# Kernel tuning notes

Measured on AMD Instinct MI355X. Metric: run time of the kernel, lower is better.

## Reference

```python
import jax, jax.numpy as jnp
import numpy as np
import math

HIDDEN, HEADS, D_K = 768, 12, 64
BS, SEQ = 4, 2048


def setup_inputs() -> dict:
    key = jax.random.key(0)
    ks = jax.random.split(key, 5)
    s = 1.0 / math.sqrt(HIDDEN)
    return {
        "x": jax.random.normal(ks[0], (BS, SEQ, HIDDEN), dtype=jnp.float32),
        "Wq": jax.random.normal(ks[1], (HIDDEN, HIDDEN), dtype=jnp.float32) * s,
        "bq": jnp.zeros((HIDDEN,), jnp.float32),
        "Wk": jax.random.normal(ks[2], (HIDDEN, HIDDEN), dtype=jnp.float32) * s,
        "bk": jnp.zeros((HIDDEN,), jnp.float32),
        "Wv": jax.random.normal(ks[3], (HIDDEN, HIDDEN), dtype=jnp.float32) * s,
        "bv": jnp.zeros((HIDDEN,), jnp.float32),
        "Wo": jax.random.normal(ks[4], (HIDDEN, HIDDEN), dtype=jnp.float32) * s,
        "bo": jnp.zeros((HIDDEN,), jnp.float32),
    }


def reference(x, Wq, bq, Wk, bk, Wv, bv, Wo, bo):
    bs, seq, _ = x.shape
    # projections; nn.Linear computes x @ W.T + b
    def proj(W, b):
        y = jnp.einsum("bsd,ed->bse", x, W) + b
        return y.reshape(bs, seq, HEADS, D_K).transpose(0, 2, 1, 3)  # [b,h,s,d]
    q, k, v = proj(Wq, bq), proj(Wk, bk), proj(Wv, bv)
    scores = jnp.einsum("bhqd,bhkd->bhqk", q, k) / jnp.sqrt(jnp.float32(D_K))
    attn = jax.nn.softmax(scores, axis=-1)  # dropout = 0 (eval)
    ctx = jnp.einsum("bhqk,bhkd->bhqd", attn, v)
    ctx = ctx.transpose(0, 2, 1, 3).reshape(bs, seq, HIDDEN)
    return jnp.einsum("bsd,ed->bse", ctx, Wo) + bo
```

## Files before the change

### kernel.cpp

```cpp
#include <hip/hip_runtime.h>
#include <hip/hip_bf16.h>

#define HID 768
#define NHEAD 12
#define DKH 64
#define BSZ 4
#define SEQ 2048
#define MTOT (BSZ*SEQ)
#define NBH (BSZ*NHEAD)

typedef __attribute__((ext_vector_type(8))) short   s16x8;
typedef __attribute__((ext_vector_type(8))) __bf16  bf16x8;
typedef __attribute__((ext_vector_type(4))) __bf16  bf16x4;
typedef __attribute__((ext_vector_type(4))) float   f32x4;

#define MFMA16x32(A,B,C) __builtin_amdgcn_mfma_f32_16x16x32_bf16((A),(B),(C),0,0,0)

__device__ __forceinline__ unsigned short f2bf(float f) {
  union { float f; unsigned int u; } a; a.f = f;
  return (unsigned short)((a.u + 0x7FFFu + ((a.u >> 16) & 1u)) >> 16);
}

__device__ __forceinline__ void gload_lds16(const unsigned short* g, unsigned short* l) {
  __builtin_amdgcn_global_load_lds((const __attribute__((address_space(1))) void*)g,
                                   (__attribute__((address_space(3))) void*)l, 16, 0, 0);
}

__global__ __launch_bounds__(256) void cvt_kernel(const float* __restrict__ src,
                                                  unsigned short* __restrict__ dst, int n) {
  int i = (blockIdx.x * 256 + threadIdx.x) * 4;
  if (i >= n) return;
  float4 v = *(const float4*)(src + i);
  ushort4 o;
  o.x = f2bf(v.x); o.y = f2bf(v.y); o.z = f2bf(v.z); o.w = f2bf(v.w);
  *(ushort4*)(dst + i) = o;
}

__global__ __launch_bounds__(256) void cvtw_kernel(const float* __restrict__ s0,
                                                   const float* __restrict__ s1,
                                                   const float* __restrict__ s2,
                                                   const float* __restrict__ s3,
                                                   unsigned short* __restrict__ dst) {
  const float* s = (blockIdx.y == 0) ? s0 : (blockIdx.y == 1) ? s1 : (blockIdx.y == 2) ? s2 : s3;
  int i = (blockIdx.x * 256 + threadIdx.x) * 4;
  float4 v = *(const float4*)(s + i);
  ushort4 o;
  o.x = f2bf(v.x); o.y = f2bf(v.y); o.z = f2bf(v.z); o.w = f2bf(v.w);
  *(ushort4*)(dst + (size_t)blockIdx.y * HID * HID + i) = o;
}

__global__ __launch_bounds__(256) void vtrans_kernel(const unsigned short* __restrict__ v,
                                                     unsigned short* __restrict__ vt) {
  __shared__ unsigned short t[64][72];
  const int head = blockIdx.x;
  const int tile = blockIdx.y;
  const int tid  = threadIdx.x;
  const int r = tid >> 2, c = (tid & 3) << 4;
  const unsigned short* src = v + ((size_t)head * SEQ + tile * 64) * DKH;
  s16x8 a0 = *(const s16x8*)(src + r * DKH + c);
  s16x8 a1 = *(const s16x8*)(src + r * DKH + c + 8);
#pragma unroll
  for (int e = 0; e < 8; ++e) {
    t[r][c + e]     = (unsigned short)a0[e];
    t[r][c + 8 + e] = (unsigned short)a1[e];
  }
  __syncthreads();
  unsigned short* dstrow = vt + (((size_t)head * 32 + tile) * 64 + r) * 64;
#pragma unroll
  for (int g = 0; g < 4; ++g) {
    const int kl = c + g * 4;
    const int slot = (kl >> 2) ^ (r & 15);
    ushort4 w;
    w.x = t[kl + 0][r]; w.y = t[kl + 1][r]; w.z = t[kl + 2][r]; w.w = t[kl + 3][r];
    *(ushort4*)(dstrow + slot * 4) = w;
  }
}

template<int MODE>
__global__ __launch_bounds__(256) void gemm_kernel(
    const unsigned short* __restrict__ A,
    const unsigned short* __restrict__ W,
    const float* __restrict__ bias0,
    const float* __restrict__ bias1,
    const float* __restrict__ bias2,
    void* __restrict__ out_raw)
{
  __shared__ unsigned short As[128*32];
  __shared__ unsigned short Bs[128*32];
  const int tid  = threadIdx.x;
  const int wave = tid >> 6, lane = tid & 63;
  const int l16  = lane & 15, lg = lane >> 4;
  const int m0   = blockIdx.x * 128, n0 = blockIdx.y * 128;
  const int wm   = (wave & 1) * 64,  wn = (wave >> 1) * 64;

  const f32x4 z4 = {0.f, 0.f, 0.f, 0.f};
  f32x4 acc[4][4];
#pragma unroll
  for (int i = 0; i < 4; ++i)
#pragma unroll
    for (int j = 0; j < 4; ++j) acc[i][j] = z4;

  const int sr = lane >> 2;
  const int sk = (lane & 3) * 8;

  for (int kt = 0; kt < HID; kt += 32) {
    __syncthreads();
#pragma unroll
    for (int i = 0; i < 2; ++i) {
      const int c = wave * 2 + i;
      gload_lds16(A + (size_t)(m0 + c*16 + sr) * HID + kt + sk, As + c*512);
      gload_lds16(W + (size_t)(n0 + c*16 + sr) * HID + kt + sk, Bs + c*512);
    }
    __syncthreads();
    bf16x8 af[4], bfr[4];
#pragma unroll
    for (int mb = 0; mb < 4; ++mb)
      af[mb] = *(const bf16x8*)(As + (wm + mb*16 + l16)*32 + lg*8);
#pragma unroll
    for (int nb = 0; nb < 4; ++nb)
      bfr[nb] = *(const bf16x8*)(Bs + (wn + nb*16 + l16)*32 + lg*8);
#pragma unroll
    for (int mb = 0; mb < 4; ++mb)
#pragma unroll
      for (int nb = 0; nb < 4; ++nb)
        acc[mb][nb] = MFMA16x32(af[mb], bfr[nb], acc[mb][nb]);
  }

  if (MODE == 0) {
    unsigned short* out = (unsigned short*)out_raw;
    const float QSCALE = 0.18033688011112042f;
#pragma unroll
    for (int nb = 0; nb < 4; ++nb) {
      const int n     = n0 + wn + nb*16 + l16;
      const int which = n / HID;
      const int e     = n - which * HID;
      const float* bp = (which == 0) ? bias0 : (which == 1) ? bias1 : bias2;
      const float bias = bp[e];
      const float scl  = (which == 0) ? QSCALE : 1.0f;
      const int h = e >> 6, d = e & 63;
#pragma unroll
      for (int mb = 0; mb < 4; ++mb)
#pragma unroll
        for (int j = 0; j < 4; ++j) {
          const int m = m0 + wm + mb*16 + lg*4 + j;
          const int b = m >> 11, s = m & (SEQ - 1);
          const float v = (acc[mb][nb][j] + bias) * scl;
          out[((((size_t)which*BSZ + b)*NHEAD + h)*SEQ + s)*DKH + d] = f2bf(v);
        }
    }
  } else {
    float* out = (float*)out_raw;
#pragma unroll
    for (int nb = 0; nb < 4; ++nb) {
      const int n = n0 + wn + nb*16 + l16;
      const float bias = bias0[n];
#pragma unroll
      for (int mb = 0; mb < 4; ++mb)
#pragma unroll
        for (int j = 0; j < 4; ++j) {
          const int m = m0 + wm + mb*16 + lg*4 + j;
          out[(size_t)m*HID + n] = acc[mb][nb][j] + bias;
        }
    }
  }
}

__global__ __launch_bounds__(256, 4) void attn_kernel(const unsigned short* __restrict__ qkv,
                                                      const unsigned short* __restrict__ vtimg,
                                                      unsigned short* __restrict__ ctx)
{
  __shared__ unsigned short Ks[2][64*64];
  __shared__ unsigned short Vs[2][64*64];
  const int tid  = threadIdx.x;
  const int wave = tid >> 6, lane = tid & 63;
  const int l16  = lane & 15, lg = lane >> 4;
  const int f   = blockIdx.x;
  const int xcd = f & 7, idx = f >> 3;
  const int bh  = xcd * 6 + (idx >> 4);
  const int qt  = idx & 15;
  const int b   = bh / NHEAD, h = bh - b * NHEAD;
  const int q0  = qt * 128 + wave * 32;

  const unsigned short* Qg = qkv + (size_t)bh * (SEQ*DKH);
  const unsigned short* Kg = qkv + (size_t)(NBH + bh) * (SEQ*DKH);

  const int srow  = lane >> 3;
  const int scolK = ((lane & 7) ^ srow) << 3;
  const unsigned short* kSrc0 = Kg + (size_t)(wave*16 + srow) * DKH + scolK;
  const unsigned short* kSrc1 = Kg + (size_t)(wave*16 + 8 + srow) * DKH + scolK;
  const unsigned short* vSrc0 = vtimg + ((size_t)bh*32*64 + wave*16 + srow) * 64 + (lane & 7) * 8;
  const unsigned short* vSrc1 = vSrc0 + 8*64;

  bf16x8 qf[2][2];
#pragma unroll
  for (int qa = 0; qa < 2; ++qa) {
    qf[qa][0] = *(const bf16x8*)(Qg + (size_t)(q0 + qa*16 + l16)*DKH + lg*8);
    qf[qa][1] = *(const bf16x8*)(Qg + (size_t)(q0 + qa*16 + l16)*DKH + 32 + lg*8);
  }

  bf16x8 ones;
#pragma unroll
  for (int e = 0; e < 8; ++e) ones[e] = (__bf16)1.0f;

  const f32x4 z4 = {0.f,0.f,0.f,0.f};
  f32x4 cacc[2][4];
  f32x4 csum[2] = {z4, z4};
#pragma unroll
  for (int qa = 0; qa < 2; ++qa)
#pragma unroll
    for (int db = 0; db < 4; ++db) cacc[qa][db] = z4;

  gload_lds16(kSrc0, Ks[0] + wave*1024);
  gload_lds16(kSrc1, Ks[0] + wave*1024 + 512);
  gload_lds16(vSrc0, Vs[0] + wave*1024);
  gload_lds16(vSrc1, Vs[0] + wave*1024 + 512);
  kSrc0 += 64*DKH; kSrc1 += 64*DKH; vSrc0 += 64*64; vSrc1 += 64*64;
  __syncthreads();

  const int NT = SEQ / 64;
  for (int t = 0; t < NT; ++t) {
    const int cur = t & 1;
    if (t + 1 < NT) {
      gload_lds16(kSrc0, Ks[cur^1] + wave*1024);
      gload_lds16(kSrc1, Ks[cur^1] + wave*1024 + 512);
      gload_lds16(vSrc0, Vs[cur^1] + wave*1024);
      gload_lds16(vSrc1, Vs[cur^1] + wave*1024 + 512);
      kSrc0 += 64*DKH; kSrc1 += 64*DKH; vSrc0 += 64*64; vSrc1 += 64*64;
    }

    const char* kb = (const char*)Ks[cur];
    f32x4 sc[2][4];
    __builtin_amdgcn_s_setprio(1);
#pragma unroll
    for (int nb = 0; nb < 4; ++nb) {
      const int kr = nb*16 + l16;
      const int sw = (kr & 7) << 4;
      bf16x8 kf0 = *(const bf16x8*)(kb + ((kr*128 + lg*16) ^ sw));
      bf16x8 kf1 = *(const bf16x8*)(kb + ((kr*128 + 64 + lg*16) ^ sw));
      f32x4 z0 = z4, z1 = z4;
      z0 = MFMA16x32(kf0, qf[0][0], z0);
      z0 = MFMA16x32(kf1, qf[0][1], z0);
      z1 = MFMA16x32(kf0, qf[1][0], z1);
      z1 = MFMA16x32(kf1, qf[1][1], z1);
      sc[0][nb] = z0; sc[1][nb] = z1;
    }
    __builtin_amdgcn_s_setprio(0);

    bf16x8 pa[2][2];
#pragma unroll
    for (int qa = 0; qa < 2; ++qa)
#pragma unroll
      for (int nb = 0; nb < 4; ++nb)
#pragma unroll
        for (int j = 0; j < 4; ++j)
          pa[qa][nb>>1][(nb&1)*4 + j] = (__bf16)__builtin_amdgcn_exp2f(sc[qa][nb][j]);

    const char* vb = (const char*)Vs[cur];
    __builtin_amdgcn_s_setprio(1);
    csum[0] = MFMA16x32(pa[0][0], ones, csum[0]);
    csum[0] = MFMA16x32(pa[0][1], ones, csum[0]);
    csum[1] = MFMA16x32(pa[1][0], ones, csum[1]);
    csum[1] = MFMA16x32(pa[1][1], ones, csum[1]);
#pragma unroll
    for (int db = 0; db < 4; ++db) {
      const int dbase = (db*16 + l16) * 128;
      bf16x4 v00 = *(const bf16x4*)(vb + dbase + (((0 | lg) ^ l16) << 3));
      bf16x4 v01 = *(const bf16x4*)(vb + dbase + (((4 | lg) ^ l16) << 3));
      bf16x4 v10 = *(const bf16x4*)(vb + dbase + (((8 | lg) ^ l16) << 3));
      bf16x4 v11 = *(const bf16x4*)(vb + dbase + (((12 | lg) ^ l16) << 3));
      bf16x8 vf0 = __builtin_shufflevector(v00, v01, 0,1,2,3,4,5,6,7);
      bf16x8 vf1 = __builtin_shufflevector(v10, v11, 0,1,2,3,4,5,6,7);
      cacc[0][db] = MFMA16x32(pa[0][0], vf0, cacc[0][db]);
      cacc[0][db] = MFMA16x32(pa[0][1], vf1, cacc[0][db]);
      cacc[1][db] = MFMA16x32(pa[1][0], vf0, cacc[1][db]);
      cacc[1][db] = MFMA16x32(pa[1][1], vf1, cacc[1][db]);
    }
    __builtin_amdgcn_s_setprio(0);

    __syncthreads();
  }

#pragma unroll
  for (int qa = 0; qa < 2; ++qa) {
    f32x4 inv;
#pragma unroll
    for (int j = 0; j < 4; ++j) inv[j] = 1.0f / csum[qa][j];
#pragma unroll
    for (int db = 0; db < 4; ++db)
#pragma unroll
      for (int j = 0; j < 4; ++j) {
        const int srow2 = q0 + qa*16 + lg*4 + j;
        ctx[((size_t)(b*SEQ + srow2))*HID + h*DKH + db*16 + l16] = f2bf(cacc[qa][db][j] * inv[j]);
      }
  }
}

extern "C" void kernel_launch(void* const* d_in, const int* in_sizes, int n_in,
                              void* d_out, int out_size, void* d_ws, size_t ws_size,
                              hipStream_t stream) {
  (void)in_sizes; (void)n_in; (void)out_size; (void)ws_size;
  const float* x  = (const float*)d_in[0];
  const float* Wq = (const float*)d_in[1];
  const float* bq = (const float*)d_in[2];
  const float* Wk = (const float*)d_in[3];
  const float* bk = (const float*)d_in[4];
  const float* Wv = (const float*)d_in[5];
  const float* bv = (const float*)d_in[6];
  const float* Wo = (const float*)d_in[7];
  const float* bo = (const float*)d_in[8];

  unsigned short* ws   = (unsigned short*)d_ws;
  unsigned short* Xb   = ws;
  unsigned short* Wqkv = Xb + (size_t)MTOT * HID;
  unsigned short* Wob  = Wqkv + (size_t)3 * HID * HID;
  unsigned short* qkvb = Wob + (size_t)HID * HID;
  unsigned short* vtb  = qkvb + (size_t)3 * NBH * SEQ * DKH;
  unsigned short* ctxb = Xb;

  cvt_kernel<<<(MTOT*HID)/1024, 256, 0, stream>>>(x, Xb, MTOT*HID);
  cvtw_kernel<<<dim3((HID*HID)/1024, 4), 256, 0, stream>>>(Wq, Wk, Wv, Wo, Wqkv);

  gemm_kernel<0><<<dim3(MTOT/128, 2304/128), 256, 0, stream>>>(Xb, Wqkv, bq, bk, bv, qkvb);
  vtrans_kernel<<<dim3(NBH, SEQ/64), 256, 0, stream>>>(qkvb + (size_t)2*NBH*SEQ*DKH, vtb);
  attn_kernel<<<768, 256, 0, stream>>>(qkvb, vtb, ctxb);
  gemm_kernel<1><<<dim3(MTOT/128, HID/128), 256, 0, stream>>>(ctxb, Wob, bo, nullptr, nullptr, d_out);
}
```

Before: 140.2 us.

## Fuse V transpose into QKV GEMM epilogue, widen GEMM K-tile, remap blocks

The QKV projection GEMM now writes the V third directly in the transposed, swizzled layout the attention kernel expects, which removes the separate transpose kernel and one round trip of V through memory. The GEMM K-tile doubles to 64 with an XOR-swizzled LDS layout, and blocks are remapped so neighbouring tiles land on the same XCD. The attention loop is unrolled by two with precomputed LDS offsets, and its launch bounds drop to 3 blocks per CU. Risks are scattered 8-byte V stores, more LDS per GEMM block, and lower attention occupancy.

```diff
diff --git a/kernel.cpp b/kernel.cpp
--- a/kernel.cpp
+++ b/kernel.cpp
@@ -49,33 +49,6 @@
   *(ushort4*)(dst + (size_t)blockIdx.y * HID * HID + i) = o;
 }
 
-__global__ __launch_bounds__(256) void vtrans_kernel(const unsigned short* __restrict__ v,
-                                                     unsigned short* __restrict__ vt) {
-  __shared__ unsigned short t[64][72];
-  const int head = blockIdx.x;
-  const int tile = blockIdx.y;
-  const int tid  = threadIdx.x;
-  const int r = tid >> 2, c = (tid & 3) << 4;
-  const unsigned short* src = v + ((size_t)head * SEQ + tile * 64) * DKH;
-  s16x8 a0 = *(const s16x8*)(src + r * DKH + c);
-  s16x8 a1 = *(const s16x8*)(src + r * DKH + c + 8);
-#pragma unroll
-  for (int e = 0; e < 8; ++e) {
-    t[r][c + e]     = (unsigned short)a0[e];
-    t[r][c + 8 + e] = (unsigned short)a1[e];
-  }
-  __syncthreads();
-  unsigned short* dstrow = vt + (((size_t)head * 32 + tile) * 64 + r) * 64;
-#pragma unroll
-  for (int g = 0; g < 4; ++g) {
-    const int kl = c + g * 4;
-    const int slot = (kl >> 2) ^ (r & 15);
-    ushort4 w;
-    w.x = t[kl + 0][r]; w.y = t[kl + 1][r]; w.z = t[kl + 2][r]; w.w = t[kl + 3][r];
-    *(ushort4*)(dstrow + slot * 4) = w;
-  }
-}
-
 template<int MODE>
 __global__ __launch_bounds__(256) void gemm_kernel(
     const unsigned short* __restrict__ A,
@@ -83,14 +56,18 @@
     const float* __restrict__ bias0,
     const float* __restrict__ bias1,
     const float* __restrict__ bias2,
-    void* __restrict__ out_raw)
+    void* __restrict__ out_raw,
+    unsigned short* __restrict__ vtimg)
 {
-  __shared__ unsigned short As[128*32];
-  __shared__ unsigned short Bs[128*32];
+  __shared__ unsigned short As[128*64];
+  __shared__ unsigned short Bs[128*64];
   const int tid  = threadIdx.x;
   const int wave = tid >> 6, lane = tid & 63;
   const int l16  = lane & 15, lg = lane >> 4;
-  const int m0   = blockIdx.x * 128, n0 = blockIdx.y * 128;
+  const int f    = blockIdx.x;
+  const int xcd  = f & 7, rr = f >> 3;
+  const int bx   = xcd*8 + (rr & 7), by = rr >> 3;
+  const int m0   = bx * 128, n0 = by * 128;
   const int wm   = (wave & 1) * 64,  wn = (wave >> 1) * 64;
 
   const f32x4 z4 = {0.f, 0.f, 0.f, 0.f};
@@ -100,53 +77,84 @@
 #pragma unroll
     for (int j = 0; j < 4; ++j) acc[i][j] = z4;
 
-  const int sr = lane >> 2;
-  const int sk = (lane & 3) * 8;
-
-  for (int kt = 0; kt < HID; kt += 32) {
+  const int sr  = lane >> 3;
+  const int sc8 = ((lane & 7) ^ sr) << 3;
+
+  for (int kt = 0; kt < HID; kt += 64) {
     __syncthreads();
 #pragma unroll
-    for (int i = 0; i < 2; ++i) {
-      const int c = wave * 2 + i;
-      gload_lds16(A + (size_t)(m0 + c*16 + sr) * HID + kt + sk, As + c*512);
-      gload_lds16(W + (size_t)(n0 + c*16 + sr) * HID + kt + sk, Bs + c*512);
+    for (int i = 0; i < 4; ++i) {
+      const int c = wave * 4 + i;
+      gload_lds16(A + (size_t)(m0 + c*8 + sr) * HID + kt + sc8, As + c*512);
+      gload_lds16(W + (size_t)(n0 + c*8 + sr) * HID + kt + sc8, Bs + c*512);
     }
     __syncthreads();
-    bf16x8 af[4], bfr[4];
-#pragma unroll
-    for (int mb = 0; mb < 4; ++mb)
-      af[mb] = *(const bf16x8*)(As + (wm + mb*16 + l16)*32 + lg*8);
-#pragma unroll
-    for (int nb = 0; nb < 4; ++nb)
-      bfr[nb] = *(const bf16x8*)(Bs + (wn + nb*16 + l16)*32 + lg*8);
-#pragma unroll
-    for (int mb = 0; mb < 4; ++mb)
-#pragma unroll
-      for (int nb = 0; nb < 4; ++nb)
-        acc[mb][nb] = MFMA16x32(af[mb], bfr[nb], acc[mb][nb]);
+    const char* ab = (const char*)As;
+    const char* bb = (const char*)Bs;
+#pragma unroll
+    for (int kk = 0; kk < 2; ++kk) {
+      bf16x8 af[4], bfr[4];
+#pragma unroll
+      for (int mb = 0; mb < 4; ++mb) {
+        const int r = wm + mb*16 + l16;
+        af[mb] = *(const bf16x8*)(ab + r*128 + (((kk*4 + lg) ^ (l16 & 7)) << 4));
+      }
+#pragma unroll
+      for (int nb = 0; nb < 4; ++nb) {
+        const int r = wn + nb*16 + l16;
+        bfr[nb] = *(const bf16x8*)(bb + r*128 + (((kk*4 + lg) ^ (l16 & 7)) << 4));
+      }
+#pragma unroll
+      for (int mb = 0; mb < 4; ++mb)
+#pragma unroll
+        for (int nb = 0; nb < 4; ++nb)
+          acc[mb][nb] = MFMA16x32(af[mb], bfr[nb], acc[mb][nb]);
+    }
   }
 
   if (MODE == 0) {
     unsigned short* out = (unsigned short*)out_raw;
     const float QSCALE = 0.18033688011112042f;
-#pragma unroll
-    for (int nb = 0; nb < 4; ++nb) {
-      const int n     = n0 + wn + nb*16 + l16;
-      const int which = n / HID;
-      const int e     = n - which * HID;
-      const float* bp = (which == 0) ? bias0 : (which == 1) ? bias1 : bias2;
-      const float bias = bp[e];
+    const int which = (n0 + wn) / HID;
+    if (which == 2) {
+      const int h = (n0 + wn - 2*HID) >> 6;
+#pragma unroll
+      for (int nb = 0; nb < 4; ++nb) {
+        const int d = nb*16 + l16;
+        const float bias = bias2[h*64 + d];
+#pragma unroll
+        for (int mb = 0; mb < 4; ++mb) {
+          const int m    = m0 + wm + mb*16 + lg*4;
+          const int b    = m >> 11, s = m & (SEQ - 1);
+          const int tile = s >> 6;
+          const int slot = ((s & 63) >> 2) ^ l16;
+          ushort4 w;
+          w.x = f2bf(acc[mb][nb][0] + bias);
+          w.y = f2bf(acc[mb][nb][1] + bias);
+          w.z = f2bf(acc[mb][nb][2] + bias);
+          w.w = f2bf(acc[mb][nb][3] + bias);
+          *(ushort4*)(vtimg + ((((size_t)(b*NHEAD + h)*32 + tile)*64 + d)*64 + slot*4)) = w;
+        }
+      }
+    } else {
+      const float* bp  = (which == 0) ? bias0 : bias1;
       const float scl  = (which == 0) ? QSCALE : 1.0f;
-      const int h = e >> 6, d = e & 63;
-#pragma unroll
-      for (int mb = 0; mb < 4; ++mb)
-#pragma unroll
-        for (int j = 0; j < 4; ++j) {
-          const int m = m0 + wm + mb*16 + lg*4 + j;
-          const int b = m >> 11, s = m & (SEQ - 1);
-          const float v = (acc[mb][nb][j] + bias) * scl;
-          out[((((size_t)which*BSZ + b)*NHEAD + h)*SEQ + s)*DKH + d] = f2bf(v);
-        }
+      const int e_base = n0 + wn - which*HID;
+#pragma unroll
+      for (int nb = 0; nb < 4; ++nb) {
+        const int e = e_base + nb*16 + l16;
+        const float bias = bp[e];
+        const int h = e >> 6, d = e & 63;
+#pragma unroll
+        for (int mb = 0; mb < 4; ++mb)
+#pragma unroll
+          for (int j = 0; j < 4; ++j) {
+            const int m = m0 + wm + mb*16 + lg*4 + j;
+            const int b = m >> 11, s = m & (SEQ - 1);
+            const float v = (acc[mb][nb][j] + bias) * scl;
+            out[((((size_t)which*BSZ + b)*NHEAD + h)*SEQ + s)*DKH + d] = f2bf(v);
+          }
+      }
     }
   } else {
     float* out = (float*)out_raw;
@@ -165,7 +173,63 @@
   }
 }
 
-__global__ __launch_bounds__(256, 4) void attn_kernel(const unsigned short* __restrict__ qkv,
+#define ATTN_STEP(CUR, DOPREF)                                              \
+  {                                                                         \
+    if (DOPREF) {                                                           \
+      gload_lds16(kSrc0, Ks[(CUR)^1] + wave*1024);                          \
+      gload_lds16(kSrc1, Ks[(CUR)^1] + wave*1024 + 512);                    \
+      gload_lds16(vSrc0, Vs[(CUR)^1] + wave*1024);                          \
+      gload_lds16(vSrc1, Vs[(CUR)^1] + wave*1024 + 512);                    \
+      kSrc0 += 64*DKH; kSrc1 += 64*DKH; vSrc0 += 4096; vSrc1 += 4096;       \
+    }                                                                       \
+    const char* kb = (const char*)Ks[CUR];                                  \
+    const char* vb = (const char*)Vs[CUR];                                  \
+    f32x4 sc[2][4];                                                         \
+    __builtin_amdgcn_s_setprio(1);                                          \
+    _Pragma("unroll")                                                       \
+    for (int nb = 0; nb < 4; ++nb) {                                        \
+      bf16x8 kf0 = *(const bf16x8*)(kb + kbase0 + nb*2048);                 \
+      bf16x8 kf1 = *(const bf16x8*)(kb + kbase1 + nb*2048);                 \
+      f32x4 z0 = z4, z1 = z4;                                               \
+      z0 = MFMA16x32(kf0, qf[0][0], z0);                                    \
+      z0 = MFMA16x32(kf1, qf[0][1], z0);                                    \
+      z1 = MFMA16x32(kf0, qf[1][0], z1);                                    \
+      z1 = MFMA16x32(kf1, qf[1][1], z1);                                    \
+      sc[0][nb] = z0; sc[1][nb] = z1;                                       \
+    }                                                                       \
+    __builtin_amdgcn_s_setprio(0);                                          \
+    bf16x8 pa[2][2];                                                        \
+    _Pragma("unroll")                                                       \
+    for (int qa = 0; qa < 2; ++qa)                                          \
+      _Pragma("unroll")                                                     \
+      for (int nb = 0; nb < 4; ++nb)                                        \
+        _Pragma("unroll")                                                   \
+        for (int j = 0; j < 4; ++j)                                         \
+          pa[qa][nb>>1][(nb&1)*4 + j] =                                     \
+            (__bf16)__builtin_amdgcn_exp2f(sc[qa][nb][j]);                  \
+    __builtin_amdgcn_s_setprio(1);                                          \
+    csum[0] = MFMA16x32(pa[0][0], ones, csum[0]);                           \
+    csum[0] = MFMA16x32(pa[0][1], ones, csum[0]);                           \
+    csum[1] = MFMA16x32(pa[1][0], ones, csum[1]);                           \
+    csum[1] = MFMA16x32(pa[1][1], ones, csum[1]);                           \
+    _Pragma("unroll")                                                       \
+    for (int db = 0; db < 4; ++db) {                                        \
+      bf16x4 v00 = *(const bf16x4*)(vb + vbase0 + db*2048);                 \
+      bf16x4 v01 = *(const bf16x4*)(vb + vbase1 + db*2048);                 \
+      bf16x4 v10 = *(const bf16x4*)(vb + vbase2 + db*2048);                 \
+      bf16x4 v11 = *(const bf16x4*)(vb + vbase3 + db*2048);                 \
+      bf16x8 vf0 = __builtin_shufflevector(v00, v01, 0,1,2,3,4,5,6,7);      \
+      bf16x8 vf1 = __builtin_shufflevector(v10, v11, 0,1,2,3,4,5,6,7);      \
+      cacc[0][db] = MFMA16x32(pa[0][0], vf0, cacc[0][db]);                  \
+      cacc[0][db] = MFMA16x32(pa[0][1], vf1, cacc[0][db]);                  \
+      cacc[1][db] = MFMA16x32(pa[1][0], vf0, cacc[1][db]);                  \
+      cacc[1][db] = MFMA16x32(pa[1][1], vf1, cacc[1][db]);                  \
+    }                                                                       \
+    __builtin_amdgcn_s_setprio(0);                                          \
+    __syncthreads();                                                        \
+  }
+
+__global__ __launch_bounds__(256, 3) void attn_kernel(const unsigned short* __restrict__ qkv,
                                                       const unsigned short* __restrict__ vtimg,
                                                       unsigned short* __restrict__ ctx)
 {
@@ -191,6 +255,13 @@
   const unsigned short* vSrc0 = vtimg + ((size_t)bh*32*64 + wave*16 + srow) * 64 + (lane & 7) * 8;
   const unsigned short* vSrc1 = vSrc0 + 8*64;
 
+  const int kbase0 = l16*128 + ((lg ^ (l16 & 7)) << 4);
+  const int kbase1 = l16*128 + (((lg + 4) ^ (l16 & 7)) << 4);
+  const int vbase0 = l16*128 + (((lg     ) ^ l16) << 3);
+  const int vbase1 = l16*128 + (((lg +  4) ^ l16) << 3);
+  const int vbase2 = l16*128 + (((lg +  8) ^ l16) << 3);
+  const int vbase3 = l16*128 + (((lg + 12) ^ l16) << 3);
+
   bf16x8 qf[2][2];
 #pragma unroll
   for (int qa = 0; qa < 2; ++qa) {
@@ -214,70 +285,13 @@
   gload_lds16(kSrc1, Ks[0] + wave*1024 + 512);
   gload_lds16(vSrc0, Vs[0] + wave*1024);
   gload_lds16(vSrc1, Vs[0] + wave*1024 + 512);
-  kSrc0 += 64*DKH; kSrc1 += 64*DKH; vSrc0 += 64*64; vSrc1 += 64*64;
+  kSrc0 += 64*DKH; kSrc1 += 64*DKH; vSrc0 += 4096; vSrc1 += 4096;
   __syncthreads();
 
-  const int NT = SEQ / 64;
-  for (int t = 0; t < NT; ++t) {
-    const int cur = t & 1;
-    if (t + 1 < NT) {
-      gload_lds16(kSrc0, Ks[cur^1] + wave*1024);
-      gload_lds16(kSrc1, Ks[cur^1] + wave*1024 + 512);
-      gload_lds16(vSrc0, Vs[cur^1] + wave*1024);
-      gload_lds16(vSrc1, Vs[cur^1] + wave*1024 + 512);
-      kSrc0 += 64*DKH; kSrc1 += 64*DKH; vSrc0 += 64*64; vSrc1 += 64*64;
-    }
-
-    const char* kb = (const char*)Ks[cur];
-    f32x4 sc[2][4];
-    __builtin_amdgcn_s_setprio(1);
-#pragma unroll
-    for (int nb = 0; nb < 4; ++nb) {
-      const int kr = nb*16 + l16;
-      const int sw = (kr & 7) << 4;
-      bf16x8 kf0 = *(const bf16x8*)(kb + ((kr*128 + lg*16) ^ sw));
-      bf16x8 kf1 = *(const bf16x8*)(kb + ((kr*128 + 64 + lg*16) ^ sw));
-      f32x4 z0 = z4, z1 = z4;
-      z0 = MFMA16x32(kf0, qf[0][0], z0);
-      z0 = MFMA16x32(kf1, qf[0][1], z0);
-      z1 = MFMA16x32(kf0, qf[1][0], z1);
-      z1 = MFMA16x32(kf1, qf[1][1], z1);
-      sc[0][nb] = z0; sc[1][nb] = z1;
-    }
-    __builtin_amdgcn_s_setprio(0);
-
-    bf16x8 pa[2][2];
-#pragma unroll
-    for (int qa = 0; qa < 2; ++qa)
-#pragma unroll
-      for (int nb = 0; nb < 4; ++nb)
-#pragma unroll
-        for (int j = 0; j < 4; ++j)
-          pa[qa][nb>>1][(nb&1)*4 + j] = (__bf16)__builtin_amdgcn_exp2f(sc[qa][nb][j]);
-
-    const char* vb = (const char*)Vs[cur];
-    __builtin_amdgcn_s_setprio(1);
-    csum[0] = MFMA16x32(pa[0][0], ones, csum[0]);
-    csum[0] = MFMA16x32(pa[0][1], ones, csum[0]);
-    csum[1] = MFMA16x32(pa[1][0], ones, csum[1]);
-    csum[1] = MFMA16x32(pa[1][1], ones, csum[1]);
-#pragma unroll
-    for (int db = 0; db < 4; ++db) {
-      const int dbase = (db*16 + l16) * 128;
-      bf16x4 v00 = *(const bf16x4*)(vb + dbase + (((0 | lg) ^ l16) << 3));
-      bf16x4 v01 = *(const bf16x4*)(vb + dbase + (((4 | lg) ^ l16) << 3));
-      bf16x4 v10 = *(const bf16x4*)(vb + dbase + (((8 | lg) ^ l16) << 3));
-      bf16x4 v11 = *(const bf16x4*)(vb + dbase + (((12 | lg) ^ l16) << 3));
-      bf16x8 vf0 = __builtin_shufflevector(v00, v01, 0,1,2,3,4,5,6,7);
-      bf16x8 vf1 = __builtin_shufflevector(v10, v11, 0,1,2,3,4,5,6,7);
-      cacc[0][db] = MFMA16x32(pa[0][0], vf0, cacc[0][db]);
-      cacc[0][db] = MFMA16x32(pa[0][1], vf1, cacc[0][db]);
-      cacc[1][db] = MFMA16x32(pa[1][0], vf0, cacc[1][db]);
-      cacc[1][db] = MFMA16x32(pa[1][1], vf1, cacc[1][db]);
-    }
-    __builtin_amdgcn_s_setprio(0);
-
-    __syncthreads();
+#pragma unroll 1
+  for (int tt = 0; tt < 16; ++tt) {
+    ATTN_STEP(0, true)
+    ATTN_STEP(1, (tt < 15))
   }
 
 #pragma unroll
@@ -314,14 +328,13 @@
   unsigned short* Wqkv = Xb + (size_t)MTOT * HID;
   unsigned short* Wob  = Wqkv + (size_t)3 * HID * HID;
   unsigned short* qkvb = Wob + (size_t)HID * HID;
-  unsigned short* vtb  = qkvb + (size_t)3 * NBH * SEQ * DKH;
+  unsigned short* vtb  = qkvb + (size_t)2 * NBH * SEQ * DKH;
   unsigned short* ctxb = Xb;
 
   cvt_kernel<<<(MTOT*HID)/1024, 256, 0, stream>>>(x, Xb, MTOT*HID);
   cvtw_kernel<<<dim3((HID*HID)/1024, 4), 256, 0, stream>>>(Wq, Wk, Wv, Wo, Wqkv);
 
-  gemm_kernel<0><<<dim3(MTOT/128, 2304/128), 256, 0, stream>>>(Xb, Wqkv, bq, bk, bv, qkvb);
-  vtrans_kernel<<<dim3(NBH, SEQ/64), 256, 0, stream>>>(qkvb + (size_t)2*NBH*SEQ*DKH, vtb);
+  gemm_kernel<0><<<1152, 256, 0, stream>>>(Xb, Wqkv, bq, bk, bv, qkvb, vtb);
   attn_kernel<<<768, 256, 0, stream>>>(qkvb, vtb, ctxb);
-  gemm_kernel<1><<<dim3(MTOT/128, HID/128), 256, 0, stream>>>(ctxb, Wob, bo, nullptr, nullptr, d_out);
-}
+  gemm_kernel<1><<<384, 256, 0, stream>>>(ctxb, Wob, bo, nullptr, nullptr, d_out, nullptr);
+}
```

Measured after the change: 135.3 us. 1.04x faster.
